# Optimization experiments

Measured on AMD Instinct MI355X. Metric: run time of the kernel, lower is better.

## Reference

```python
import jax, jax.numpy as jnp
import numpy as np

# Graph sizes: each graph has exactly 32 nodes (forced by the rearrange + lin1 in_features)
BS = 4096
NODES = 32
N = BS * NODES          # 131072 total nodes
F_IN = 128
E_PER_G = 512
E = BS * E_PER_G        # 2097152 edges, all within-graph
HID = 1024
NCLS = 10


def setup_inputs() -> dict:
    key = jax.random.key(0)
    ks = jax.random.split(key, 9)
    x = jax.random.normal(ks[0], (N, F_IN), dtype=jnp.float32)
    # within-graph random edges: local node ids in [0,32) + per-graph offset
    graph_off = jnp.repeat(jnp.arange(BS, dtype=jnp.int64), E_PER_G) * NODES
    src = jax.random.randint(ks[1], (E,), 0, NODES, dtype=jnp.int64) + graph_off
    dst = jax.random.randint(ks[2], (E,), 0, NODES, dtype=jnp.int64) + graph_off
    edge_index = jnp.stack([src, dst], axis=0)
    s = 0.05
    gconv_w = jax.random.normal(ks[3], (F_IN, F_IN), dtype=jnp.float32) * s
    gconv_b = jax.random.normal(ks[4], (F_IN,), dtype=jnp.float32) * s
    lin1_w = jax.random.normal(ks[5], (HID, F_IN * NODES), dtype=jnp.float32) * s
    lin1_b = jax.random.normal(ks[6], (HID,), dtype=jnp.float32) * s
    lin2_w = jax.random.normal(ks[7], (NCLS, HID), dtype=jnp.float32) * s
    lin2_b = jax.random.normal(ks[8], (NCLS,), dtype=jnp.float32) * s
    return {"x": x, "edge_index": edge_index, "gconv_w": gconv_w,
            "gconv_b": gconv_b, "lin1_w": lin1_w, "lin1_b": lin1_b,
            "lin2_w": lin2_w, "lin2_b": lin2_b, "bs": BS}


def reference(x, edge_index, gconv_w, gconv_b, lin1_w, lin1_b, lin2_w, lin2_b, bs):
    # GINConv (eps=0): h_i = Linear( x_i + sum_{j->i} x_j )
    src, dst = edge_index[0], edge_index[1]
    agg = jax.ops.segment_sum(x[src], dst, num_segments=x.shape[0])  # [N, F]
    h = (x + agg) @ gconv_w.T + gconv_b                               # [N, F]
    h = jax.nn.relu(h)
    # rearrange '(bs e) f -> bs (f e)' with e=32 nodes per graph
    f = h.shape[-1]
    h = h.reshape(bs, NODES, f).transpose(0, 2, 1).reshape(bs, f * NODES)
    h = h @ lin1_w.T + lin1_b
    # dropout is identity in eval mode
    h = jax.nn.relu(h)
    h = h @ lin2_w.T + lin2_b
    return jax.nn.softmax(h, axis=-1)
```

## Files before the change

### kernel.cpp

```cpp
#include <hip/hip_runtime.h>

typedef _Float16 half_t;
typedef _Float16 halfv8 __attribute__((ext_vector_type(8)));
typedef _Float16 halfv4 __attribute__((ext_vector_type(4)));
typedef float    floatv4 __attribute__((ext_vector_type(4)));
typedef unsigned int uint;
typedef uint uintv4 __attribute__((ext_vector_type(4)));

#define NODES 32
#define FIN   128
#define EPG   512
#define NBS   4096
#define ETOT  (NBS*EPG)
#define HID   1024
#define KDIM  4096
#define NCLS  10
#define WPITCH 136
#define YPITCH 36

#define BM 256
#define BN 256
#define BK 64
#define KS 4
#define KSLEN (KDIM/KS)
#define NT (KSLEN/BK)

#define GLDS16(g, l)                                                        \
  __builtin_amdgcn_global_load_lds(                                         \
      (const __attribute__((address_space(1))) unsigned int*)(g),           \
      (__attribute__((address_space(3))) unsigned int*)(l), 16, 0, 0)

__global__ __launch_bounds__(256) void prep_w1(const float* __restrict__ w1,
                                               half_t* __restrict__ w1p) {
  __shared__ float tmp[FIN * 33];
  const int o = blockIdx.x, t = threadIdx.x;
  const floatv4* src = (const floatv4*)(w1 + (size_t)o * KDIM);
  for (int i = t; i < KDIM / 4; i += 256) {
    floatv4 v = src[i];
    const int f = i >> 3;
    const int n = (i & 7) * 4;
#pragma unroll
    for (int q = 0; q < 4; ++q) tmp[f * 33 + n + q] = v[q];
  }
  __syncthreads();
  half_t* dst = w1p + (size_t)o * KDIM;
  for (int i = t; i < KDIM; i += 256) {
    const int n = i >> 7, f = i & 127;
    dst[i] = (half_t)tmp[f * 33 + n];
  }
}

__global__ __launch_bounds__(256, 2) void gin_fused(
    const float* __restrict__ x, const int* __restrict__ ei,
    const float* __restrict__ gw, const float* __restrict__ gb,
    half_t* __restrict__ H) {
  __shared__ __attribute__((aligned(16))) half_t Ws[FIN * WPITCH];
  __shared__ __attribute__((aligned(16))) half_t Yt[4][FIN * YPITCH];
  __shared__ __attribute__((aligned(16))) uint  cnt[4][512];

  const int t = threadIdx.x, w = t >> 6, l = t & 63;
  const int lr = l & 15, lk = l >> 4;
  const int g = blockIdx.x * 4 + w;

  const float* xg = x + (size_t)g * (NODES * FIN);
  floatv4 xr[2][4][2];
#pragma unroll
  for (int mt = 0; mt < 2; ++mt)
#pragma unroll
    for (int kk = 0; kk < 4; ++kk) {
      const float* p = xg + (mt * 16 + lr) * FIN + kk * 32 + lk * 8;
      xr[mt][kk][0] = *(const floatv4*)p;
      xr[mt][kk][1] = *(const floatv4*)(p + 4);
    }
  const int* sp = ei + (size_t)g * EPG;
  const int* dp = ei + (size_t)ETOT + (size_t)g * EPG;
  uintv4 s0 = *(const uintv4*)(sp + l * 8);
  uintv4 s1 = *(const uintv4*)(sp + l * 8 + 4);
  uintv4 d0 = *(const uintv4*)(dp + l * 8);
  uintv4 d1 = *(const uintv4*)(dp + l * 8 + 4);

  {
    uintv4* c4 = (uintv4*)cnt[w];
    uintv4 z = {0, 0, 0, 0};
    c4[l] = z;
    c4[l + 64] = z;
  }
  for (int i = t; i < (FIN * FIN) / 4; i += 256) {
    const int o = i >> 5, kc = (i & 31) * 4;
    floatv4 v = *(const floatv4*)(gw + o * FIN + kc);
    halfv4 h = {(half_t)v[0], (half_t)v[1], (half_t)v[2], (half_t)v[3]};
    *(halfv4*)&Ws[o * WPITCH + kc] = h;
  }
  __syncthreads();

#pragma unroll
  for (int q = 0; q < 4; ++q) {
    uint p0 = (d0[q] & 31) * 32 + (s0[q] & 31);
    atomicAdd(&cnt[w][p0 >> 1], 1u << ((p0 & 1) * 16));
    uint p1 = (d1[q] & 31) * 32 + (s1[q] & 31);
    atomicAdd(&cnt[w][p1 >> 1], 1u << ((p1 & 1) * 16));
  }

  halfv8 af[2][4];
#pragma unroll
  for (int mt = 0; mt < 2; ++mt)
#pragma unroll
    for (int kk = 0; kk < 4; ++kk) {
      halfv8 h;
#pragma unroll
      for (int q = 0; q < 4; ++q) {
        h[q]     = (half_t)xr[mt][kk][0][q];
        h[q + 4] = (half_t)xr[mt][kk][1][q];
      }
      af[mt][kk] = h;
    }

  floatv4 acc[2][8] = {};
#pragma unroll
  for (int kk = 0; kk < 4; ++kk)
#pragma unroll
    for (int nt = 0; nt < 8; ++nt) {
      halfv8 bf = *(const halfv8*)&Ws[(nt * 16 + lr) * WPITCH + kk * 32 + lk * 8];
#pragma unroll
      for (int mt = 0; mt < 2; ++mt)
        acc[mt][nt] = __builtin_amdgcn_mfma_f32_16x16x32_f16(af[mt][kk], bf,
                                                             acc[mt][nt], 0, 0, 0);
    }

  half_t* yw = Yt[w];
#pragma unroll
  for (int mt = 0; mt < 2; ++mt)
#pragma unroll
    for (int nt = 0; nt < 8; ++nt) {
      halfv4 h = {(half_t)acc[mt][nt][0], (half_t)acc[mt][nt][1],
                  (half_t)acc[mt][nt][2], (half_t)acc[mt][nt][3]};
      *(halfv4*)&yw[(nt * 16 + lr) * YPITCH + mt * 16 + lk * 4] = h;
    }

  const unsigned short* c16 = (const unsigned short*)cnt[w];
  halfv8 am[2];
#pragma unroll
  for (int mt = 0; mt < 2; ++mt) {
    const int i = mt * 16 + lr;
#pragma unroll
    for (int q = 0; q < 8; ++q) {
      const int j = lk * 8 + q;
      float c = (float)c16[i * 32 + j] + ((j == i) ? 1.f : 0.f);
      am[mt][q] = (half_t)c;
    }
  }

  floatv4 acc2[2][8] = {};
#pragma unroll
  for (int nt = 0; nt < 8; ++nt) {
    halfv8 bf = *(const halfv8*)&yw[(nt * 16 + lr) * YPITCH + lk * 8];
#pragma unroll
    for (int mt = 0; mt < 2; ++mt)
      acc2[mt][nt] = __builtin_amdgcn_mfma_f32_16x16x32_f16(am[mt], bf,
                                                            acc2[mt][nt], 0, 0, 0);
  }

  half_t* Hg = H + (size_t)g * KDIM;
#pragma unroll
  for (int nt = 0; nt < 8; ++nt) {
    const float bias = gb[nt * 16 + lr];
#pragma unroll
    for (int mt = 0; mt < 2; ++mt)
#pragma unroll
      for (int q = 0; q < 4; ++q) {
        const int m = mt * 16 + lk * 4 + q;
        const float v = acc2[mt][nt][q] + bias;
        Hg[m * FIN + nt * 16 + lr] = (half_t)(v > 0.f ? v : 0.f);
      }
  }
}

__global__ __launch_bounds__(512, 2) void lin1_gemm(
    const half_t* __restrict__ A, const half_t* __restrict__ B,
    half_t* __restrict__ Cbase) {
  __shared__ __attribute__((aligned(16))) half_t As[2][BM * BK];
  __shared__ __attribute__((aligned(16))) half_t Bs[2][BN * BK];

  const int t = threadIdx.x;
  const int orig = blockIdx.x;
  const int wg = (orig & 7) * 32 + (orig >> 3);
  const int mt = wg & 15, rest = wg >> 4;
  const int nt_ = rest & 3, ks = rest >> 2;
  const int m0 = mt * BM, n0 = nt_ * BN, k0 = ks * KSLEN;

  const half_t* gA[4];
  const half_t* gB[4];
#pragma unroll
  for (int j = 0; j < 4; ++j) {
    const int L = t + j * 512;
    const int r = L >> 3;
    const int c = (L & 7) ^ (r & 7);
    gA[j] = A + (size_t)(m0 + r) * KDIM + k0 + c * 8;
    gB[j] = B + (size_t)(n0 + r) * KDIM + k0 + c * 8;
  }

#define STAGE(buf, koff)                                                    \
  {                                                                         \
    _Pragma("unroll")                                                       \
    for (int j = 0; j < 4; ++j)                                             \
      GLDS16(gA[j] + (koff), &As[buf][(t + j * 512) * 8]);                  \
    _Pragma("unroll")                                                       \
    for (int j = 0; j < 4; ++j)                                             \
      GLDS16(gB[j] + (koff), &Bs[buf][(t + j * 512) * 8]);                  \
  }

  const int w = t >> 6, l = t & 63, lr = l & 15, lk = l >> 4;
  const int wm = (w >> 2) * 128, wn = (w & 3) * 64;

  floatv4 acc[8][4] = {};

  STAGE(0, 0)
  STAGE(1, BK)
  asm volatile("s_waitcnt vmcnt(8)" ::: "memory");
  __builtin_amdgcn_s_barrier();

  for (int kt = 0; kt < NT; ++kt) {
    const int cur = kt & 1;
    const half_t* as = As[cur];
    const half_t* bs = Bs[cur];
#pragma unroll
    for (int ksb = 0; ksb < 2; ++ksb) {
      halfv8 bf[4], af[8];
#pragma unroll
      for (int nf = 0; nf < 4; ++nf) {
        const int row = wn + nf * 16 + lr;
        const int ch = (ksb * 4 + lk) ^ (row & 7);
        bf[nf] = *(const halfv8*)&bs[row * BK + ch * 8];
      }
#pragma unroll
      for (int mf = 0; mf < 8; ++mf) {
        const int row = wm + mf * 16 + lr;
        const int ch = (ksb * 4 + lk) ^ (row & 7);
        af[mf] = *(const halfv8*)&as[row * BK + ch * 8];
      }
      __builtin_amdgcn_s_setprio(1);
#pragma unroll
      for (int mf = 0; mf < 8; ++mf)
#pragma unroll
        for (int nf = 0; nf < 4; ++nf)
          acc[mf][nf] = __builtin_amdgcn_mfma_f32_16x16x32_f16(
              af[mf], bf[nf], acc[mf][nf], 0, 0, 0);
      __builtin_amdgcn_s_setprio(0);
    }
    __builtin_amdgcn_s_barrier();
    const int src = (kt + 2 < NT) ? (kt + 2) : 0;
    STAGE(cur, src * BK)
    asm volatile("s_waitcnt vmcnt(8)" ::: "memory");
    __builtin_amdgcn_s_barrier();
  }

  half_t* C = Cbase + (size_t)ks * ((size_t)NBS * HID);
#pragma unroll
  for (int mf = 0; mf < 8; ++mf)
#pragma unroll
    for (int nf = 0; nf < 4; ++nf) {
      const int n = n0 + wn + nf * 16 + lr;
#pragma unroll
      for (int q = 0; q < 4; ++q) {
        const int m = m0 + wm + mf * 16 + lk * 4 + q;
        C[(size_t)m * HID + n] = (half_t)acc[mf][nf][q];
      }
    }
#undef STAGE
}

__global__ __launch_bounds__(256) void head(
    const half_t* __restrict__ Cb, const float* __restrict__ b1,
    const float* __restrict__ w2, const float* __restrict__ b2,
    float* __restrict__ out) {
  __shared__ __attribute__((aligned(16))) float w2s[NCLS * HID];
  const int t = threadIdx.x;
  {
    const floatv4* s4 = (const floatv4*)w2;
    floatv4* d4 = (floatv4*)w2s;
    for (int i = t; i < (NCLS * HID) / 4; i += 256) d4[i] = s4[i];
  }
  __syncthreads();
  const int w = t >> 6, l = t & 63;
  const int row = blockIdx.x * 4 + w;

  float r[16];
#pragma unroll
  for (int jj = 0; jj < 4; ++jj) {
    floatv4 bb = *(const floatv4*)&b1[jj * 256 + l * 4];
    float s[4] = {bb[0], bb[1], bb[2], bb[3]};
#pragma unroll
    for (int p = 0; p < KS; ++p) {
      const half_t* cp = Cb + (size_t)p * ((size_t)NBS * HID) + (size_t)row * HID;
      halfv4 u = *(const halfv4*)&cp[jj * 256 + l * 4];
#pragma unroll
      for (int q = 0; q < 4; ++q) s[q] += (float)u[q];
    }
#pragma unroll
    for (int q = 0; q < 4; ++q) r[jj * 4 + q] = s[q] > 0.f ? s[q] : 0.f;
  }
  float lg[10];
#pragma unroll
  for (int c = 0; c < NCLS; ++c) {
    float p = 0.f;
#pragma unroll
    for (int jj = 0; jj < 4; ++jj) {
      floatv4 wv = *(const floatv4*)&w2s[c * HID + jj * 256 + l * 4];
      p += r[jj * 4 + 0] * wv[0] + r[jj * 4 + 1] * wv[1] +
           r[jj * 4 + 2] * wv[2] + r[jj * 4 + 3] * wv[3];
    }
#pragma unroll
    for (int off = 32; off >= 1; off >>= 1) p += __shfl_xor(p, off);
    lg[c] = p + b2[c];
  }
  float mx = lg[0];
#pragma unroll
  for (int c = 1; c < NCLS; ++c) mx = fmaxf(mx, lg[c]);
  float sum = 0.f;
#pragma unroll
  for (int c = 0; c < NCLS; ++c) { lg[c] = __expf(lg[c] - mx); sum += lg[c]; }
  const float inv = 1.f / sum;
  float myv = 0.f;
#pragma unroll
  for (int c = 0; c < NCLS; ++c) myv = (l == c) ? lg[c] * inv : myv;
  if (l < NCLS) out[(size_t)row * NCLS + l] = myv;
}

extern "C" void kernel_launch(void* const* d_in, const int* in_sizes, int n_in,
                              void* d_out, int out_size, void* d_ws, size_t ws_size,
                              hipStream_t stream) {
  (void)in_sizes; (void)n_in; (void)out_size; (void)ws_size;
  const float* x  = (const float*)d_in[0];
  const int*   ei = (const int*)d_in[1];
  const float* gw = (const float*)d_in[2];
  const float* gb = (const float*)d_in[3];
  const float* w1 = (const float*)d_in[4];
  const float* b1 = (const float*)d_in[5];
  const float* w2 = (const float*)d_in[6];
  const float* b2 = (const float*)d_in[7];
  float* out = (float*)d_out;

  char* ws = (char*)d_ws;
  half_t* H   = (half_t*)(ws);
  half_t* w1p = (half_t*)(ws + 33554432);
  half_t* C   = (half_t*)(ws + 33554432 + 8388608);

  prep_w1  <<<dim3(HID),     dim3(256), 0, stream>>>(w1, w1p);
  gin_fused<<<dim3(NBS / 4), dim3(256), 0, stream>>>(x, ei, gw, gb, H);
  lin1_gemm<<<dim3(16 * 4 * KS), dim3(512), 0, stream>>>(H, w1p, C);
  head     <<<dim3(NBS / 4), dim3(256), 0, stream>>>(C, b1, w2, b2, out);
}
```

Before: 92.54 us.

## Pre-convert GIN weight to fp16 and read B fragments from global, dropping LDS copy

The fp16 conversion of the 128x128 GIN weight moves into the prep kernel, which already runs once per call, and the result is written to workspace. gin_fused no longer stages the weight into LDS each block. It loads B fragments directly from the global/L2-resident fp16 copy and drops a __syncthreads. Freeing about 34KB of LDS per block allows raising launch bounds to 3 blocks per SM, at the cost of more global/L2 traffic and register pressure from the prefetched fragments.

```diff
diff --git a/kernel.cpp b/kernel.cpp
--- a/kernel.cpp
+++ b/kernel.cpp
@@ -15,7 +15,6 @@
 #define HID   1024
 #define KDIM  4096
 #define NCLS  10
-#define WPITCH 136
 #define YPITCH 36
 
 #define BM 256
@@ -31,9 +30,15 @@
       (__attribute__((address_space(3))) unsigned int*)(l), 16, 0, 0)
 
 __global__ __launch_bounds__(256) void prep_w1(const float* __restrict__ w1,
-                                               half_t* __restrict__ w1p) {
+                                               half_t* __restrict__ w1p,
+                                               const float* __restrict__ gw,
+                                               half_t* __restrict__ gw16) {
   __shared__ float tmp[FIN * 33];
   const int o = blockIdx.x, t = threadIdx.x;
+  if (t < 16) {
+    const int i = o * 16 + t;
+    gw16[i] = (half_t)gw[i];
+  }
   const floatv4* src = (const floatv4*)(w1 + (size_t)o * KDIM);
   for (int i = t; i < KDIM / 4; i += 256) {
     floatv4 v = src[i];
@@ -50,11 +55,10 @@
   }
 }
 
-__global__ __launch_bounds__(256, 2) void gin_fused(
+__global__ __launch_bounds__(256, 3) void gin_fused(
     const float* __restrict__ x, const int* __restrict__ ei,
-    const float* __restrict__ gw, const float* __restrict__ gb,
+    const half_t* __restrict__ gw16, const float* __restrict__ gb,
     half_t* __restrict__ H) {
-  __shared__ __attribute__((aligned(16))) half_t Ws[FIN * WPITCH];
   __shared__ __attribute__((aligned(16))) half_t Yt[4][FIN * YPITCH];
   __shared__ __attribute__((aligned(16))) uint  cnt[4][512];
 
@@ -85,14 +89,6 @@
     c4[l] = z;
     c4[l + 64] = z;
   }
-  for (int i = t; i < (FIN * FIN) / 4; i += 256) {
-    const int o = i >> 5, kc = (i & 31) * 4;
-    floatv4 v = *(const floatv4*)(gw + o * FIN + kc);
-    halfv4 h = {(half_t)v[0], (half_t)v[1], (half_t)v[2], (half_t)v[3]};
-    *(halfv4*)&Ws[o * WPITCH + kc] = h;
-  }
-  __syncthreads();
-
 #pragma unroll
   for (int q = 0; q < 4; ++q) {
     uint p0 = (d0[q] & 31) * 32 + (s0[q] & 31);
@@ -117,15 +113,18 @@
 
   floatv4 acc[2][8] = {};
 #pragma unroll
-  for (int kk = 0; kk < 4; ++kk)
-#pragma unroll
-    for (int nt = 0; nt < 8; ++nt) {
-      halfv8 bf = *(const halfv8*)&Ws[(nt * 16 + lr) * WPITCH + kk * 32 + lk * 8];
+  for (int kk = 0; kk < 4; ++kk) {
+    halfv8 bfk[8];
+#pragma unroll
+    for (int nt = 0; nt < 8; ++nt)
+      bfk[nt] = *(const halfv8*)(gw16 + (nt * 16 + lr) * FIN + kk * 32 + lk * 8);
+#pragma unroll
+    for (int nt = 0; nt < 8; ++nt)
 #pragma unroll
       for (int mt = 0; mt < 2; ++mt)
-        acc[mt][nt] = __builtin_amdgcn_mfma_f32_16x16x32_f16(af[mt][kk], bf,
+        acc[mt][nt] = __builtin_amdgcn_mfma_f32_16x16x32_f16(af[mt][kk], bfk[nt],
                                                              acc[mt][nt], 0, 0, 0);
-    }
+  }
 
   half_t* yw = Yt[w];
 #pragma unroll
@@ -341,12 +340,13 @@
   float* out = (float*)d_out;
 
   char* ws = (char*)d_ws;
-  half_t* H   = (half_t*)(ws);
-  half_t* w1p = (half_t*)(ws + 33554432);
-  half_t* C   = (half_t*)(ws + 33554432 + 8388608);
-
-  prep_w1  <<<dim3(HID),     dim3(256), 0, stream>>>(w1, w1p);
-  gin_fused<<<dim3(NBS / 4), dim3(256), 0, stream>>>(x, ei, gw, gb, H);
+  half_t* H    = (half_t*)(ws);
+  half_t* w1p  = (half_t*)(ws + 33554432);
+  half_t* C    = (half_t*)(ws + 33554432 + 8388608);
+  half_t* gw16 = (half_t*)(ws + 33554432 + 8388608 + (size_t)KS * NBS * HID * 2);
+
+  prep_w1  <<<dim3(HID),     dim3(256), 0, stream>>>(w1, w1p, gw, gw16);
+  gin_fused<<<dim3(NBS / 4), dim3(256), 0, stream>>>(x, ei, gw16, gb, H);
   lin1_gemm<<<dim3(16 * 4 * KS), dim3(512), 0, stream>>>(H, w1p, C);
   head     <<<dim3(NBS / 4), dim3(256), 0, stream>>>(C, b1, w2, b2, out);
 }
```

New measurement: 94.97 us. 2.6% more time.

## Pipeline GIN kernel over 8 graphs per block with async LDS staging

Applied to the files above, without the earlier changes.

The GIN kernel now has each 256-thread block process 8 graphs in sequence instead of one graph per wave. The x tile is double-buffered in LDS via global_load_lds with an XOR swizzle, and edge indices are prefetched ahead. Output features are split across the four waves, so the 128x128 weight is converted into LDS once per block instead of once per 4 graphs. H is now stored in feature-major (f, node) order, which lets prep_w1's transpose shrink to a plain fp32→fp16 conversion. This trades more barriers and tricky vmcnt waits for less redundant weight staging and overlapped loads.

```diff
diff --git a/kernel.cpp b/kernel.cpp
--- a/kernel.cpp
+++ b/kernel.cpp
@@ -15,8 +15,9 @@
 #define HID   1024
 #define KDIM  4096
 #define NCLS  10
-#define WPITCH 136
-#define YPITCH 36
+#define WP    140
+#define YTP   36
+#define GPB   8
 
 #define BM 256
 #define BN 256
@@ -30,149 +31,168 @@
       (const __attribute__((address_space(1))) unsigned int*)(g),           \
       (__attribute__((address_space(3))) unsigned int*)(l), 16, 0, 0)
 
-__global__ __launch_bounds__(256) void prep_w1(const float* __restrict__ w1,
-                                               half_t* __restrict__ w1p) {
-  __shared__ float tmp[FIN * 33];
-  const int o = blockIdx.x, t = threadIdx.x;
-  const floatv4* src = (const floatv4*)(w1 + (size_t)o * KDIM);
-  for (int i = t; i < KDIM / 4; i += 256) {
-    floatv4 v = src[i];
-    const int f = i >> 3;
-    const int n = (i & 7) * 4;
-#pragma unroll
-    for (int q = 0; q < 4; ++q) tmp[f * 33 + n + q] = v[q];
-  }
-  __syncthreads();
-  half_t* dst = w1p + (size_t)o * KDIM;
-  for (int i = t; i < KDIM; i += 256) {
-    const int n = i >> 7, f = i & 127;
-    dst[i] = (half_t)tmp[f * 33 + n];
-  }
-}
-
-__global__ __launch_bounds__(256, 2) void gin_fused(
+__global__ __launch_bounds__(256) void prep_cvt(const float* __restrict__ w1,
+                                                half_t* __restrict__ w1p) {
+  const size_t q = (size_t)blockIdx.x * 256 + threadIdx.x;
+  floatv4 v = *(const floatv4*)(w1 + q * 4);
+  halfv4 h = {(half_t)v[0], (half_t)v[1], (half_t)v[2], (half_t)v[3]};
+  *(halfv4*)(w1p + q * 4) = h;
+}
+
+__global__ __launch_bounds__(256) void gin_fused(
     const float* __restrict__ x, const int* __restrict__ ei,
     const float* __restrict__ gw, const float* __restrict__ gb,
     half_t* __restrict__ H) {
-  __shared__ __attribute__((aligned(16))) half_t Ws[FIN * WPITCH];
-  __shared__ __attribute__((aligned(16))) half_t Yt[4][FIN * YPITCH];
-  __shared__ __attribute__((aligned(16))) uint  cnt[4][512];
+  __shared__ __attribute__((aligned(16))) half_t Ws[FIN * WP];
+  __shared__ __attribute__((aligned(16))) float  Xs[2][4096];
+  __shared__ __attribute__((aligned(16))) half_t Yt[FIN * YTP];
+  __shared__ uint cnt[2][512];
 
   const int t = threadIdx.x, w = t >> 6, l = t & 63;
   const int lr = l & 15, lk = l >> 4;
-  const int g = blockIdx.x * 4 + w;
-
-  const float* xg = x + (size_t)g * (NODES * FIN);
-  floatv4 xr[2][4][2];
-#pragma unroll
-  for (int mt = 0; mt < 2; ++mt)
-#pragma unroll
-    for (int kk = 0; kk < 4; ++kk) {
-      const float* p = xg + (mt * 16 + lr) * FIN + kk * 32 + lk * 8;
-      xr[mt][kk][0] = *(const floatv4*)p;
-      xr[mt][kk][1] = *(const floatv4*)(p + 4);
-    }
-  const int* sp = ei + (size_t)g * EPG;
-  const int* dp = ei + (size_t)ETOT + (size_t)g * EPG;
-  uintv4 s0 = *(const uintv4*)(sp + l * 8);
-  uintv4 s1 = *(const uintv4*)(sp + l * 8 + 4);
-  uintv4 d0 = *(const uintv4*)(dp + l * 8);
-  uintv4 d1 = *(const uintv4*)(dp + l * 8 + 4);
-
-  {
-    uintv4* c4 = (uintv4*)cnt[w];
-    uintv4 z = {0, 0, 0, 0};
-    c4[l] = z;
-    c4[l + 64] = z;
-  }
+  const int g0 = blockIdx.x * GPB;
+  const int* spb = ei + (size_t)g0 * EPG;
+  const int* dpb = ei + (size_t)ETOT + (size_t)g0 * EPG;
+
+#define STAGE_X(buf, gg)                                                     \
+  {                                                                          \
+    const float* xg = x + (size_t)(g0 + (gg)) * (NODES * FIN);               \
+    _Pragma("unroll")                                                        \
+    for (int i = 0; i < 4; ++i) {                                            \
+      const int p = i * 256 + t;                                             \
+      const int r = p >> 5, c = p & 31;                                      \
+      const int cs = (c & ~7) | ((c & 7) ^ (r & 7));                         \
+      GLDS16(xg + r * FIN + cs * 4, &Xs[buf][p * 4]);                        \
+    }                                                                        \
+  }
+
+  STAGE_X(0, 0)
+  __builtin_amdgcn_sched_barrier(0);
+  int2 es0 = *(const int2*)(spb + 2 * t);
+  int2 ed0 = *(const int2*)(dpb + 2 * t);
+  cnt[0][t] = 0; cnt[0][t + 256] = 0;
+  cnt[1][t] = 0; cnt[1][t + 256] = 0;
   for (int i = t; i < (FIN * FIN) / 4; i += 256) {
     const int o = i >> 5, kc = (i & 31) * 4;
     floatv4 v = *(const floatv4*)(gw + o * FIN + kc);
     halfv4 h = {(half_t)v[0], (half_t)v[1], (half_t)v[2], (half_t)v[3]};
-    *(halfv4*)&Ws[o * WPITCH + kc] = h;
+    *(halfv4*)&Ws[o * WP + kc] = h;
   }
   __syncthreads();
-
-#pragma unroll
-  for (int q = 0; q < 4; ++q) {
-    uint p0 = (d0[q] & 31) * 32 + (s0[q] & 31);
-    atomicAdd(&cnt[w][p0 >> 1], 1u << ((p0 & 1) * 16));
-    uint p1 = (d1[q] & 31) * 32 + (s1[q] & 31);
-    atomicAdd(&cnt[w][p1 >> 1], 1u << ((p1 & 1) * 16));
-  }
-
-  halfv8 af[2][4];
-#pragma unroll
-  for (int mt = 0; mt < 2; ++mt)
+  {
+    uint p0 = ((uint)ed0.x & 31) * 32 + ((uint)es0.x & 31);
+    atomicAdd(&cnt[0][p0 >> 1], 1u << ((p0 & 1) * 16));
+    uint p1 = ((uint)ed0.y & 31) * 32 + ((uint)es0.y & 31);
+    atomicAdd(&cnt[0][p1 >> 1], 1u << ((p1 & 1) * 16));
+  }
+  int2 esN = *(const int2*)(spb + EPG + 2 * t);
+  int2 edN = *(const int2*)(dpb + EPG + 2 * t);
+  const float bias0 = gb[w * 32 + lr];
+  const float bias1 = gb[w * 32 + 16 + lr];
+  asm volatile("s_waitcnt vmcnt(2)" ::: "memory");
+  __syncthreads();
+
+  for (int g = 0; g < GPB; ++g) {
+    const int cur = g & 1, nxt = cur ^ 1;
+    if (g + 1 < GPB) {
+      STAGE_X(nxt, g + 1)
+      __builtin_amdgcn_sched_barrier(0);
+      cnt[nxt][t] = 0; cnt[nxt][t + 256] = 0;
+    }
+    halfv8 af[2][4];
+#pragma unroll
+    for (int mt = 0; mt < 2; ++mt)
+#pragma unroll
+      for (int kk = 0; kk < 4; ++kk) {
+        const int r = mt * 16 + lr;
+        floatv4 u = *(const floatv4*)&Xs[cur][(r * 32 + kk * 8 + ((lk * 2 + 0) ^ (lr & 7))) * 4];
+        floatv4 v = *(const floatv4*)&Xs[cur][(r * 32 + kk * 8 + ((lk * 2 + 1) ^ (lr & 7))) * 4];
+        halfv8 h;
+#pragma unroll
+        for (int q = 0; q < 4; ++q) {
+          h[q]     = (half_t)u[q];
+          h[q + 4] = (half_t)v[q];
+        }
+        af[mt][kk] = h;
+      }
+    __syncthreads();
+    if (g + 1 < GPB) {
+      uint p0 = ((uint)edN.x & 31) * 32 + ((uint)esN.x & 31);
+      atomicAdd(&cnt[nxt][p0 >> 1], 1u << ((p0 & 1) * 16));
+      uint p1 = ((uint)edN.y & 31) * 32 + ((uint)esN.y & 31);
+      atomicAdd(&cnt[nxt][p1 >> 1], 1u << ((p1 & 1) * 16));
+    }
+    floatv4 acc[2][2] = {};
 #pragma unroll
     for (int kk = 0; kk < 4; ++kk) {
-      halfv8 h;
-#pragma unroll
-      for (int q = 0; q < 4; ++q) {
-        h[q]     = (half_t)xr[mt][kk][0][q];
-        h[q + 4] = (half_t)xr[mt][kk][1][q];
-      }
-      af[mt][kk] = h;
-    }
-
-  floatv4 acc[2][8] = {};
-#pragma unroll
-  for (int kk = 0; kk < 4; ++kk)
-#pragma unroll
-    for (int nt = 0; nt < 8; ++nt) {
-      halfv8 bf = *(const halfv8*)&Ws[(nt * 16 + lr) * WPITCH + kk * 32 + lk * 8];
+      halfv8 bf[2];
+#pragma unroll
+      for (int nt = 0; nt < 2; ++nt)
+        bf[nt] = *(const halfv8*)&Ws[(w * 32 + nt * 16 + lr) * WP + kk * 32 + lk * 8];
+#pragma unroll
+      for (int nt = 0; nt < 2; ++nt)
+#pragma unroll
+        for (int mt = 0; mt < 2; ++mt)
+          acc[mt][nt] = __builtin_amdgcn_mfma_f32_16x16x32_f16(
+              af[mt][kk], bf[nt], acc[mt][nt], 0, 0, 0);
+    }
+    if (g + 2 < GPB) {
+      esN = *(const int2*)(spb + (size_t)(g + 2) * EPG + 2 * t);
+      edN = *(const int2*)(dpb + (size_t)(g + 2) * EPG + 2 * t);
+    }
+    const unsigned short* c16 = (const unsigned short*)cnt[cur];
+    halfv8 am[2];
+#pragma unroll
+    for (int mt = 0; mt < 2; ++mt) {
+      const int i = mt * 16 + lr;
+#pragma unroll
+      for (int q = 0; q < 8; ++q) {
+        const int j = lk * 8 + q;
+        float c = (float)c16[i * 32 + j] + ((j == i) ? 1.f : 0.f);
+        am[mt][q] = (half_t)c;
+      }
+    }
+    __builtin_amdgcn_sched_barrier(0);
+#pragma unroll
+    for (int mt = 0; mt < 2; ++mt)
+#pragma unroll
+      for (int nt = 0; nt < 2; ++nt) {
+        halfv4 h = {(half_t)acc[mt][nt][0], (half_t)acc[mt][nt][1],
+                    (half_t)acc[mt][nt][2], (half_t)acc[mt][nt][3]};
+        *(halfv4*)&Yt[(w * 32 + nt * 16 + lr) * YTP + mt * 16 + lk * 4] = h;
+      }
+    __builtin_amdgcn_sched_barrier(0);
+    floatv4 acc2[2][2] = {};
+#pragma unroll
+    for (int nt = 0; nt < 2; ++nt) {
+      halfv8 bf2 = *(const halfv8*)&Yt[(w * 32 + nt * 16 + lr) * YTP + lk * 8];
 #pragma unroll
       for (int mt = 0; mt < 2; ++mt)
-        acc[mt][nt] = __builtin_amdgcn_mfma_f32_16x16x32_f16(af[mt][kk], bf,
-                                                             acc[mt][nt], 0, 0, 0);
-    }
-
-  half_t* yw = Yt[w];
-#pragma unroll
-  for (int mt = 0; mt < 2; ++mt)
-#pragma unroll
-    for (int nt = 0; nt < 8; ++nt) {
-      halfv4 h = {(half_t)acc[mt][nt][0], (half_t)acc[mt][nt][1],
-                  (half_t)acc[mt][nt][2], (half_t)acc[mt][nt][3]};
-      *(halfv4*)&yw[(nt * 16 + lr) * YPITCH + mt * 16 + lk * 4] = h;
-    }
-
-  const unsigned short* c16 = (const unsigned short*)cnt[w];
-  halfv8 am[2];
-#pragma unroll
-  for (int mt = 0; mt < 2; ++mt) {
-    const int i = mt * 16 + lr;
-#pragma unroll
-    for (int q = 0; q < 8; ++q) {
-      const int j = lk * 8 + q;
-      float c = (float)c16[i * 32 + j] + ((j == i) ? 1.f : 0.f);
-      am[mt][q] = (half_t)c;
-    }
-  }
-
-  floatv4 acc2[2][8] = {};
-#pragma unroll
-  for (int nt = 0; nt < 8; ++nt) {
-    halfv8 bf = *(const halfv8*)&yw[(nt * 16 + lr) * YPITCH + lk * 8];
-#pragma unroll
-    for (int mt = 0; mt < 2; ++mt)
-      acc2[mt][nt] = __builtin_amdgcn_mfma_f32_16x16x32_f16(am[mt], bf,
-                                                            acc2[mt][nt], 0, 0, 0);
-  }
-
-  half_t* Hg = H + (size_t)g * KDIM;
-#pragma unroll
-  for (int nt = 0; nt < 8; ++nt) {
-    const float bias = gb[nt * 16 + lr];
-#pragma unroll
-    for (int mt = 0; mt < 2; ++mt)
-#pragma unroll
-      for (int q = 0; q < 4; ++q) {
-        const int m = mt * 16 + lk * 4 + q;
-        const float v = acc2[mt][nt][q] + bias;
-        Hg[m * FIN + nt * 16 + lr] = (half_t)(v > 0.f ? v : 0.f);
-      }
-  }
+        acc2[mt][nt] = __builtin_amdgcn_mfma_f32_16x16x32_f16(
+            am[mt], bf2, acc2[mt][nt], 0, 0, 0);
+    }
+    half_t* Hg = H + (size_t)(g0 + g) * KDIM;
+#pragma unroll
+    for (int nt = 0; nt < 2; ++nt) {
+      const float bias = nt ? bias1 : bias0;
+      const int o = w * 32 + nt * 16 + lr;
+#pragma unroll
+      for (int mt = 0; mt < 2; ++mt) {
+        halfv4 h;
+#pragma unroll
+        for (int q = 0; q < 4; ++q) {
+          const float v = acc2[mt][nt][q] + bias;
+          h[q] = (half_t)(v > 0.f ? v : 0.f);
+        }
+        *(halfv4*)(Hg + o * 32 + mt * 16 + lk * 4) = h;
+      }
+    }
+    if (g + 1 < GPB) {
+      asm volatile("s_waitcnt vmcnt(6)" ::: "memory");
+      __syncthreads();
+    }
+  }
+#undef STAGE_X
 }
 
 __global__ __launch_bounds__(512, 2) void lin1_gemm(
@@ -342,11 +362,11 @@
 
   char* ws = (char*)d_ws;
   half_t* H   = (half_t*)(ws);
-  half_t* w1p = (half_t*)(ws + 33554432);
-  half_t* C   = (half_t*)(ws + 33554432 + 8388608);
-
-  prep_w1  <<<dim3(HID),     dim3(256), 0, stream>>>(w1, w1p);
-  gin_fused<<<dim3(NBS / 4), dim3(256), 0, stream>>>(x, ei, gw, gb, H);
+  half_t* C   = (half_t*)(ws + 33554432);
+  half_t* w1p = (half_t*)(ws + 67108864);
+
+  prep_cvt <<<dim3(4096),      dim3(256), 0, stream>>>(w1, w1p);
+  gin_fused<<<dim3(NBS / GPB), dim3(256), 0, stream>>>(x, ei, gw, gb, H);
   lin1_gemm<<<dim3(16 * 4 * KS), dim3(512), 0, stream>>>(H, w1p, C);
-  head     <<<dim3(NBS / 4), dim3(256), 0, stream>>>(C, b1, w2, b2, out);
-}
+  head     <<<dim3(NBS / 4),   dim3(256), 0, stream>>>(C, b1, w2, b2, out);
+}
```

New measurement: 90.15 us. 1.03x faster.
